# Kernel optimization log

Hardware: AMD Instinct MI355X
Metric: run time of the kernel (lower is better)

Reference implementation:

```python
import jax, jax.numpy as jnp
import numpy as np

DIM = 384
HEADS = 12
HEAD_DIM = DIM // HEADS
SCALE = HEAD_DIM ** -0.5
HIDDEN = 4 * DIM
EPS = 1e-5


def _dwconv(x, w, b):
    # depthwise 3x3 conv, NCHW, kernel [C,1,3,3], groups=C
    y = jax.lax.conv_general_dilated(
        x, w, window_strides=(1, 1), padding='SAME',
        dimension_numbers=('NCHW', 'OIHW', 'NCHW'),
        feature_group_count=x.shape[1])
    return y + b[None, :, None, None]


def _layernorm(x, g, b):
    mu = jnp.mean(x, axis=-1, keepdims=True)
    var = jnp.mean(jnp.square(x - mu), axis=-1, keepdims=True)
    return (x - mu) * jax.lax.rsqrt(var + EPS) * g + b


def setup_inputs() -> dict:
    key = jax.random.key(0)
    ks = jax.random.split(key, 10)
    s = 0.02
    inp = {
        'x': jax.random.normal(ks[0], (32, DIM, 28, 28), dtype=jnp.float32),
        'cpe1_w': jax.random.normal(ks[1], (DIM, 1, 3, 3), dtype=jnp.float32) * s,
        'cpe1_b': jnp.zeros((DIM,), jnp.float32),
        'norm1_g': jnp.ones((DIM,), jnp.float32),
        'norm1_b': jnp.zeros((DIM,), jnp.float32),
        'qkv_w': jax.random.normal(ks[2], (3 * DIM, DIM), dtype=jnp.float32) * s,
        'proj_w': jax.random.normal(ks[3], (DIM, DIM), dtype=jnp.float32) * s,
        'proj_b': jnp.zeros((DIM,), jnp.float32),
        'cpe2_w': jax.random.normal(ks[4], (DIM, 1, 3, 3), dtype=jnp.float32) * s,
        'cpe2_b': jnp.zeros((DIM,), jnp.float32),
        'norm2_g': jnp.ones((DIM,), jnp.float32),
        'norm2_b': jnp.zeros((DIM,), jnp.float32),
        'fc1_w': jax.random.normal(ks[5], (HIDDEN, DIM), dtype=jnp.float32) * s,
        'fc1_b': jnp.zeros((HIDDEN,), jnp.float32),
        'fc2_w': jax.random.normal(ks[6], (DIM, HIDDEN), dtype=jnp.float32) * s,
        'fc2_b': jnp.zeros((DIM,), jnp.float32),
    }
    return inp


def reference(x, cpe1_w, cpe1_b, norm1_g, norm1_b, qkv_w, proj_w, proj_b,
              cpe2_w, cpe2_b, norm2_g, norm2_b, fc1_w, fc1_b, fc2_w, fc2_b):
    B, C, H, W = x.shape
    N = H * W
    # cpe1: depthwise conv residual (act = Identity)
    x = x + _dwconv(x, cpe1_w, cpe1_b)
    x = jnp.transpose(x.reshape(B, C, N), (0, 2, 1))  # [B, N, C]

    # channel attention
    cur = _layernorm(x, norm1_g, norm1_b)
    qkv = cur @ qkv_w.T  # [B, N, 3C]
    qkv = qkv.reshape(B, N, 3, HEADS, HEAD_DIM)
    q = qkv[:, :, 0]  # [B, N, h, d]
    k = qkv[:, :, 1] * SCALE
    v = qkv[:, :, 2]
    # attn = k^T @ v over tokens: [B, h, d, d]
    attn = jnp.einsum('bnhd,bnhe->bhde', k, v)
    attn = jax.nn.softmax(attn, axis=-1)
    # out[n,d] = sum_e attn[d,e] * q[n,e]
    out = jnp.einsum('bhde,bnhe->bnhd', attn, q).reshape(B, N, C)
    cur = out @ proj_w.T + proj_b
    x = x + cur

    # cpe2
    x = jnp.transpose(x, (0, 2, 1)).reshape(B, C, H, W)
    x = x + _dwconv(x, cpe2_w, cpe2_b)

    # MLP
    x = jnp.transpose(x.reshape(B, C, N), (0, 2, 1))  # [B, N, C]
    y = _layernorm(x, norm2_g, norm2_b)
    y = jax.nn.gelu(y @ fc1_w.T + fc1_b, approximate=False)
    y = y @ fc2_w.T + fc2_b
    x = x + y
    return jnp.transpose(x, (0, 2, 1)).reshape(B, C, H, W)
```

## Files before the change

kernel.cpp:

```cpp
#include <hip/hip_runtime.h>
#include <hip/hip_bf16.h>

#define CDIM 384
#define NHEADS 12
#define HDIM 32
#define HIDDEN 1536
#define BBATCH 32
#define HH 28
#define WW 28
#define NTOK 784
#define BN (BBATCH * NTOK)
#define LN_EPS 1e-5f
#define ATT_SCALE 0.17677669529663687f
#define YTILES 196
#define PERXCD 25

typedef __hip_bfloat16 bf16;
typedef __attribute__((ext_vector_type(8))) short bf16x8;
typedef __attribute__((ext_vector_type(4))) float f32x4;

__device__ __forceinline__ float ldf(const float* p) { return *p; }
__device__ __forceinline__ float ldf(const bf16* p) { return __bfloat162float(*p); }
__device__ __forceinline__ void stf(float* p, float v) { *p = v; }
__device__ __forceinline__ void stf(bf16* p, float v) { *p = __float2bfloat16(v); }

__device__ __forceinline__ short f2bs(float v) {
    bf16 t = __float2bfloat16(v);
    return *reinterpret_cast<short*>(&t);
}

__device__ __forceinline__ float gelu_f(float x) {
    float u = x * (0.7978845608f + 0.0356774081f * x * x);
    float e = __expf(-2.f * u);
    return x / (1.f + e);
}

__device__ __forceinline__ void gload16(const void* g, void* l) {
    __builtin_amdgcn_global_load_lds(
        (const __attribute__((address_space(1))) unsigned int*)g,
        (__attribute__((address_space(3))) unsigned int*)l, 16, 0, 0);
}

__global__ __launch_bounds__(256) void f2b4_k(
    const float* __restrict__ w0, const float* __restrict__ w1,
    const float* __restrict__ w2, const float* __restrict__ w3,
    bf16* __restrict__ dst)
{
    int i = blockIdx.x * 256 + threadIdx.x;
    const float* src; int off;
    if (i < 442368)       { src = w0; off = i; }
    else if (i < 589824)  { src = w1; off = i - 442368; }
    else if (i < 1179648) { src = w2; off = i - 589824; }
    else                  { src = w3; off = i - 1179648; }
    dst[i] = __float2bfloat16(src[off]);
}

__global__ __launch_bounds__(256) void wtr_k(const float* __restrict__ w,
                                             float* __restrict__ wt)
{
    int i = blockIdx.x * 256 + threadIdx.x;
    if (i < 9 * CDIM) {
        int k = i / CDIM, c = i % CDIM;
        wt[i] = w[c * 9 + k];
    }
}

__global__ __launch_bounds__(256) void dwconv_nchw_plane(
    const float* __restrict__ x, const float* __restrict__ w,
    const float* __restrict__ bias, float* __restrict__ y)
{
    __shared__ float sm[NTOK];
    int bc = blockIdx.x;
    int c = bc % CDIM;
    const float* xp = x + (size_t)bc * NTOK;
    int tid = threadIdx.x;
#pragma unroll
    for (int i = 0; i < 4; i++) {
        int p = tid + i * 256;
        if (p < NTOK) sm[p] = xp[p];
    }
    __syncthreads();
    const float* wp = w + c * 9;
    float w00 = wp[0], w01 = wp[1], w02 = wp[2];
    float w10 = wp[3], w11 = wp[4], w12 = wp[5];
    float w20 = wp[6], w21 = wp[7], w22 = wp[8];
    float bc_ = bias[c];
    float* yp = y + (size_t)bc * NTOK;
#pragma unroll
    for (int i = 0; i < 4; i++) {
        int p = tid + i * 256;
        if (p >= NTOK) break;
        int h = p / WW, wcol = p % WW;
        bool hm = h > 0, hp = h < HH - 1, wm = wcol > 0, wpv = wcol < WW - 1;
        float s = w11 * sm[p];
        if (hm)        s += w01 * sm[p - WW];
        if (hp)        s += w21 * sm[p + WW];
        if (wm)        s += w10 * sm[p - 1];
        if (wpv)       s += w12 * sm[p + 1];
        if (hm && wm)  s += w00 * sm[p - WW - 1];
        if (hm && wpv) s += w02 * sm[p - WW + 1];
        if (hp && wm)  s += w20 * sm[p + WW - 1];
        if (hp && wpv) s += w22 * sm[p + WW + 1];
        yp[p] = sm[p] + s + bc_;
    }
}

__global__ __launch_bounds__(256) void transpose_in(
    const float* __restrict__ in, float* __restrict__ out)
{
    __shared__ float t[32][33];
    int b = blockIdx.z;
    int n0 = blockIdx.y * 32;
    int c0 = blockIdx.x * 32;
    int tx = threadIdx.x, ty = threadIdx.y;
    for (int i = ty; i < 32; i += 8) {
        int n = n0 + tx;
        if (n < NTOK) t[i][tx] = in[((size_t)b * CDIM + c0 + i) * NTOK + n];
    }
    __syncthreads();
    for (int i = ty; i < 32; i += 8) {
        int n = n0 + i;
        if (n < NTOK) out[((size_t)b * NTOK + n) * CDIM + c0 + tx] = t[tx][i];
    }
}

__global__ __launch_bounds__(256) void dwconv_bnc_v2(
    const float* __restrict__ xin, const float* __restrict__ wt,
    const float* __restrict__ bias, float* __restrict__ xout)
{
    const int nblk = (BN * 96) / 256;
    const int per = nblk >> 3;
    int blk = blockIdx.x;
    int blk2 = (blk & 7) * per + (blk >> 3);
    int g4 = blk2 * 256 + threadIdx.x;
    int q = g4 % 96;
    int r = g4 / 96;
    int c = q * 4;
    int n = r % NTOK, b = r / NTOK;
    int h = n / WW, wcol = n % WW;
    const float4* base = (const float4*)(xin + (size_t)b * NTOK * CDIM);
    bool hm = h > 0, hp = h < HH - 1, wm = wcol > 0, wpv = wcol < WW - 1;

    float4 ctr = base[(size_t)n * 96 + q];
    float4 acc = {0.f, 0.f, 0.f, 0.f};

    const float4* w4 = (const float4*)wt;
#define TAP(k, cond, dn)                                            \
    if (cond) {                                                     \
        float4 vv = base[(size_t)(n + (dn)) * 96 + q];              \
        float4 ww = w4[(k) * 96 + q];                               \
        acc.x = fmaf(ww.x, vv.x, acc.x);                            \
        acc.y = fmaf(ww.y, vv.y, acc.y);                            \
        acc.z = fmaf(ww.z, vv.z, acc.z);                            \
        acc.w = fmaf(ww.w, vv.w, acc.w);                            \
    }
    TAP(0, hm && wm,   -WW - 1)
    TAP(1, hm,         -WW)
    TAP(2, hm && wpv,  -WW + 1)
    TAP(3, wm,         -1)
    { float4 ww = w4[4 * 96 + q];
      acc.x = fmaf(ww.x, ctr.x, acc.x); acc.y = fmaf(ww.y, ctr.y, acc.y);
      acc.z = fmaf(ww.z, ctr.z, acc.z); acc.w = fmaf(ww.w, ctr.w, acc.w); }
    TAP(5, wpv,        1)
    TAP(6, hp && wm,   WW - 1)
    TAP(7, hp,         WW)
    TAP(8, hp && wpv,  WW + 1)
#undef TAP
    float4 bb = *(const float4*)(bias + c);
    float4 outv;
    outv.x = ctr.x + acc.x + bb.x;
    outv.y = ctr.y + acc.y + bb.y;
    outv.z = ctr.z + acc.z + bb.z;
    outv.w = ctr.w + acc.w + bb.w;
    ((float4*)(xout))[g4] = outv;
}

template <typename TO>
__global__ __launch_bounds__(256) void layernorm_k(
    const float* __restrict__ in, const float* __restrict__ g,
    const float* __restrict__ b, TO* __restrict__ out)
{
    int wid = threadIdx.x >> 6;
    int lane = threadIdx.x & 63;
    size_t r = (size_t)blockIdx.x * 4 + wid;
    const float* row = in + r * CDIM;
    float v[6];
    float s = 0.f;
#pragma unroll
    for (int j = 0; j < 6; j++) { v[j] = row[lane + 64 * j]; s += v[j]; }
#pragma unroll
    for (int off = 32; off >= 1; off >>= 1) s += __shfl_xor(s, off);
    float mu = s * (1.f / CDIM);
    float q = 0.f;
#pragma unroll
    for (int j = 0; j < 6; j++) { float d = v[j] - mu; q += d * d; }
#pragma unroll
    for (int off = 32; off >= 1; off >>= 1) q += __shfl_xor(q, off);
    float rs = rsqrtf(q * (1.f / CDIM) + LN_EPS);
    TO* orow = out + r * CDIM;
#pragma unroll
    for (int j = 0; j < 6; j++) {
        int c = lane + 64 * j;
        stf(&orow[c], (v[j] - mu) * rs * g[c] + b[c]);
    }
}

template <int ACT, bool RES, typename TO>
__global__ __launch_bounds__(256, 4) void gemm_mfma(
    const short* __restrict__ Abf, const short* __restrict__ Bw,
    const float* __restrict__ bias, const float* __restrict__ res,
    TO* __restrict__ Co, int K, int M, int NX)
{
    int id = blockIdx.x;
    int xcd = id & 7, slot_ = id >> 3;
    int yloc = slot_ / NX, xx = slot_ - yloc * NX;
    int y = xcd * PERXCD + yloc;
    if (y >= YTILES) return;

    __shared__ __align__(16) short lds[16896];
    const int tid = threadIdx.x;
    const int wid = tid >> 6, lane = tid & 63;
    const int wrow = wid >> 1, wcol = wid & 1;
    const int quad = lane >> 4, lr = lane & 15;
    const int r0 = y * 128, m0 = xx * 128;

    const int srow = lane >> 2;
    const int sg   = (lane & 3) ^ (lane >> 4);
    const short* gA = Abf + (size_t)(r0 + wid * 32 + srow) * K + sg * 8;
    const short* gB = Bw  + (size_t)(m0 + wid * 32 + srow) * K + sg * 8;

    auto stage = [&](int k0, int p) {
        short* lA = lds + p * 8192 + wid * 1024;
        short* lB = lds + p * 8192 + 4096 + wid * 1024;
#pragma unroll
        for (int k = 0; k < 2; k++) {
            gload16(gA + k0 + (size_t)k * 16 * K, lA + k * 512);
            gload16(gB + k0 + (size_t)k * 16 * K, lB + k * 512);
        }
    };

    const int slot = (quad ^ (lr >> 2)) * 8;
    int fAoff[4], fBoff[4];
#pragma unroll
    for (int i = 0; i < 4; i++) {
        fAoff[i] = (wrow * 64 + i * 16 + lr) * 32 + slot;
        fBoff[i] = (wcol * 64 + i * 16 + lr) * 32 + slot;
    }

    f32x4 acc[4][4] = {};

    stage(0, 0);
    int p = 0;
    for (int k0 = 0; k0 < K; k0 += 32) {
        __syncthreads();
        if (k0 + 32 < K) stage(k0 + 32, p ^ 1);
        const short* As = lds + p * 8192;
        const short* Bs = As + 4096;
        bf16x8 av[4], bv[4];
#pragma unroll
        for (int i = 0; i < 4; i++) {
            av[i] = *(const bf16x8*)(As + fAoff[i]);
            bv[i] = *(const bf16x8*)(Bs + fBoff[i]);
        }
#pragma unroll
        for (int i = 0; i < 4; i++)
#pragma unroll
            for (int j = 0; j < 4; j++)
                acc[i][j] = __builtin_amdgcn_mfma_f32_16x16x32_bf16(
                    av[i], bv[j], acc[i][j], 0, 0, 0);
        p ^= 1;
    }

    if constexpr (sizeof(TO) == 4) {
#pragma unroll
        for (int i = 0; i < 4; i++) {
            int gr = r0 + wrow * 64 + i * 16 + quad * 4;
#pragma unroll
            for (int j = 0; j < 4; j++) {
                int gc = m0 + wcol * 64 + j * 16 + lr;
                float bb = bias ? bias[gc] : 0.f;
#pragma unroll
                for (int rr = 0; rr < 4; rr++) {
                    size_t idx = (size_t)(gr + rr) * M + gc;
                    float v = acc[i][j][rr] + bb;
                    if (RES) v += res[idx];
                    if (ACT == 1) v = gelu_f(v);
                    stf((float*)&Co[idx], v);
                }
            }
        }
    } else {
        __syncthreads();
        short* Cs = lds;
#pragma unroll
        for (int i = 0; i < 4; i++) {
            int lrow = wrow * 64 + i * 16 + quad * 4;
#pragma unroll
            for (int j = 0; j < 4; j++) {
                int lcol = wcol * 64 + j * 16 + lr;
                float bb = bias ? bias[m0 + lcol] : 0.f;
#pragma unroll
                for (int rr = 0; rr < 4; rr++) {
                    float v = acc[i][j][rr] + bb;
                    if (ACT == 1) v = gelu_f(v);
                    Cs[(lrow + rr) * 132 + lcol] = f2bs(v);
                }
            }
        }
        __syncthreads();
        short* co = (short*)Co;
#pragma unroll
        for (int s = 0; s < 16; s++) {
            int row = s * 8 + (tid >> 5);
            int seg = tid & 31;
            uint2 vv = *(const uint2*)(Cs + row * 132 + seg * 4);
            *(uint2*)(co + (size_t)(r0 + row) * M + m0 + seg * 4) = vv;
        }
    }
}

__global__ __launch_bounds__(256) void attn_k(
    const bf16* __restrict__ qkv, float* __restrict__ attn)
{
    int bh = blockIdx.x;
    int b = bh / NHEADS, h = bh % NHEADS;
    __shared__ float ks[64][32];
    __shared__ float vs[64][32];
    __shared__ float sm[32][33];
    int tid = threadIdx.x;
    int d = tid >> 3, e0 = (tid & 7) * 4;
    float acc[4] = {0.f, 0.f, 0.f, 0.f};
    for (int n0 = 0; n0 < NTOK; n0 += 64) {
#pragma unroll
        for (int i = 0; i < 8; i++) {
            int idx = tid + i * 256;
            int nn = idx >> 5, cc = idx & 31;
            int n = n0 + nn;
            float kv = 0.f, vv = 0.f;
            if (n < NTOK) {
                size_t base = ((size_t)b * NTOK + n) * (3 * CDIM);
                kv = ATT_SCALE * __bfloat162float(qkv[base + CDIM + h * HDIM + cc]);
                vv = __bfloat162float(qkv[base + 2 * CDIM + h * HDIM + cc]);
            }
            ks[nn][cc] = kv; vs[nn][cc] = vv;
        }
        __syncthreads();
#pragma unroll 8
        for (int nn = 0; nn < 64; nn++) {
            float kd = ks[nn][d];
#pragma unroll
            for (int j = 0; j < 4; j++) acc[j] += kd * vs[nn][e0 + j];
        }
        __syncthreads();
    }
#pragma unroll
    for (int j = 0; j < 4; j++) sm[d][e0 + j] = acc[j];
    __syncthreads();
    if (tid < 32) {
        float mx = -1e30f;
#pragma unroll
        for (int e = 0; e < 32; e++) mx = fmaxf(mx, sm[tid][e]);
        float ssum = 0.f;
        float ex[32];
#pragma unroll
        for (int e = 0; e < 32; e++) { ex[e] = expf(sm[tid][e] - mx); ssum += ex[e]; }
        float inv = 1.f / ssum;
        float* arow = attn + ((size_t)bh * 32 + tid) * 32;
#pragma unroll
        for (int e = 0; e < 32; e++) arow[e] = ex[e] * inv;
    }
}

__global__ __launch_bounds__(384) void apply_attn_k(
    const bf16* __restrict__ qkv, const float* __restrict__ attn,
    bf16* __restrict__ out)
{
    int b = blockIdx.x;
    int chunk = blockIdx.y;
    int tid = threadIdx.x;
    int h = tid >> 5;
    __shared__ float qs[8][CDIM];
    float at[32];
    const float4* ap = (const float4*)(attn + ((size_t)(b * NHEADS) * 32 + tid) * 32);
#pragma unroll
    for (int e4 = 0; e4 < 8; e4++) {
        float4 v = ap[e4];
        at[e4 * 4 + 0] = v.x; at[e4 * 4 + 1] = v.y;
        at[e4 * 4 + 2] = v.z; at[e4 * 4 + 3] = v.w;
    }
    int nbase = chunk * 56;
    for (int t0 = 0; t0 < 56; t0 += 8) {
        __syncthreads();
#pragma unroll
        for (int i = 0; i < 8; i++) {
            int n = nbase + t0 + i;
            qs[i][tid] = __bfloat162float(qkv[((size_t)b * NTOK + n) * (3 * CDIM) + tid]);
        }
        __syncthreads();
#pragma unroll
        for (int i = 0; i < 8; i++) {
            const float* qrow = &qs[i][h * 32];
            float s = 0.f;
#pragma unroll
            for (int e = 0; e < 32; e++) s += at[e] * qrow[e];
            int n = nbase + t0 + i;
            out[((size_t)b * NTOK + n) * CDIM + tid] = __float2bfloat16(s);
        }
    }
}

__global__ __launch_bounds__(256) void transpose_out(
    const float* __restrict__ in, float* __restrict__ out)
{
    __shared__ float t[32][33];
    int b = blockIdx.z;
    int n0 = blockIdx.y * 32;
    int c0 = blockIdx.x * 32;
    int tx = threadIdx.x, ty = threadIdx.y;
    for (int i = ty; i < 32; i += 8) {
        int n = n0 + i;
        if (n < NTOK) t[i][tx] = in[((size_t)b * NTOK + n) * CDIM + c0 + tx];
    }
    __syncthreads();
    for (int i = ty; i < 32; i += 8) {
        int c = c0 + i;
        int n = n0 + tx;
        if (n < NTOK) out[((size_t)b * CDIM + c) * NTOK + n] = t[tx][i];
    }
}

extern "C" void kernel_launch(void* const* d_in, const int* in_sizes, int n_in,
                              void* d_out, int out_size, void* d_ws, size_t ws_size,
                              hipStream_t stream) {
    const float* x      = (const float*)d_in[0];
    const float* cpe1_w = (const float*)d_in[1];
    const float* cpe1_b = (const float*)d_in[2];
    const float* n1g    = (const float*)d_in[3];
    const float* n1b    = (const float*)d_in[4];
    const float* qkv_w  = (const float*)d_in[5];
    const float* proj_w = (const float*)d_in[6];
    const float* proj_b = (const float*)d_in[7];
    const float* cpe2_w = (const float*)d_in[8];
    const float* cpe2_b = (const float*)d_in[9];
    const float* n2g    = (const float*)d_in[10];
    const float* n2b    = (const float*)d_in[11];
    const float* fc1_w  = (const float*)d_in[12];
    const float* fc1_b  = (const float*)d_in[13];
    const float* fc2_w  = (const float*)d_in[14];
    const float* fc2_b  = (const float*)d_in[15];

    const size_t A = (size_t)BN * CDIM;
    const size_t HA = A / 2;

    bf16* wqkv  = (bf16*)d_ws;
    bf16* wproj = wqkv + 442368;
    bf16* wfc1  = wproj + 147456;
    bf16* wfc2  = wfc1 + 589824;
    float* base = (float*)d_ws + 884736;

    float* xt        = base;
    bf16*  curb      = (bf16*)(base + A);
    bf16*  ylnb      = (bf16*)(base + A);
    bf16*  qkvb      = (bf16*)(base + A + HA);
    float* x3        = base + A + HA;
    bf16*  h1        = (bf16*)(base + A + HA + A);
    float* attnm     = base + 3 * A;
    bf16*  attn_outb = (bf16*)(base + 3 * A + 393216);
    float* finalb    = base;
    float* xconv     = base + (A * 7) / 2;
    float* cpe2_wt   = base + (A * 9) / 2;

    const int GEMM_GRID3  = 8 * PERXCD * 3;
    const int GEMM_GRID9  = 8 * PERXCD * 9;
    const int GEMM_GRID12 = 8 * PERXCD * 12;

    f2b4_k<<<1769472 / 256, 256, 0, stream>>>(qkv_w, proj_w, fc1_w, fc2_w, wqkv);
    wtr_k<<<14, 256, 0, stream>>>(cpe2_w, cpe2_wt);

    dwconv_nchw_plane<<<BBATCH * CDIM, 256, 0, stream>>>(x, cpe1_w, cpe1_b, xconv);
    transpose_in<<<dim3(CDIM / 32, (NTOK + 31) / 32, BBATCH), dim3(32, 8), 0, stream>>>(
        xconv, xt);
    layernorm_k<bf16><<<BN / 4, 256, 0, stream>>>(xt, n1g, n1b, curb);
    gemm_mfma<0, false, bf16><<<GEMM_GRID9, 256, 0, stream>>>(
        (const short*)curb, (const short*)wqkv, nullptr, nullptr, qkvb, 384, 1152, 9);
    attn_k<<<BBATCH * NHEADS, 256, 0, stream>>>(qkvb, attnm);
    apply_attn_k<<<dim3(BBATCH, 14), 384, 0, stream>>>(qkvb, attnm, attn_outb);
    gemm_mfma<0, true, float><<<GEMM_GRID3, 256, 0, stream>>>(
        (const short*)attn_outb, (const short*)wproj, proj_b, xt, xt, 384, 384, 3);
    dwconv_bnc_v2<<<(BN * 96) / 256, 256, 0, stream>>>(xt, cpe2_wt, cpe2_b, x3);
    layernorm_k<bf16><<<BN / 4, 256, 0, stream>>>(x3, n2g, n2b, ylnb);
    gemm_mfma<1, false, bf16><<<GEMM_GRID12, 256, 0, stream>>>(
        (const short*)ylnb, (const short*)wfc1, fc1_b, nullptr, h1, 384, 1536, 12);
    gemm_mfma<0, true, float><<<GEMM_GRID3, 256, 0, stream>>>(
        (const short*)h1, (const short*)wfc2, fc2_b, x3, finalb, 1536, 384, 3);
    transpose_out<<<dim3(CDIM / 32, (NTOK + 31) / 32, BBATCH), dim3(32, 8), 0, stream>>>(
        finalb, (float*)d_out);
}
```

Measured before the change: 451.2 us.

## Fuse cpe2 with layernorm, fold output transpose into fc2 GEMM epilogue

Merges the depthwise cpe2 conv with layernorm2 into one kernel that stages the conv weights in LDS, and writes the fc2 GEMM output directly in NCHW through an LDS-staged transposed epilogue, which removes the transpose_out kernel. It also merges the two weight-prep kernels, makes K a template constant, changes the LDS swizzle pattern, and vectorises the inner loops of the attention kernels with float4. The aim is to cut kernel launches and full-tensor round trips through global memory. In exchange, the transposed epilogue adds LDS passes and barriers, and the fused conv reads neighbouring token rows without coalescing them across threads.

```diff
diff --git a/kernel.cpp b/kernel.cpp
--- a/kernel.cpp
+++ b/kernel.cpp
@@ -19,8 +19,6 @@
 typedef __attribute__((ext_vector_type(8))) short bf16x8;
 typedef __attribute__((ext_vector_type(4))) float f32x4;
 
-__device__ __forceinline__ float ldf(const float* p) { return *p; }
-__device__ __forceinline__ float ldf(const bf16* p) { return __bfloat162float(*p); }
 __device__ __forceinline__ void stf(float* p, float v) { *p = v; }
 __device__ __forceinline__ void stf(bf16* p, float v) { *p = __float2bfloat16(v); }
 
@@ -41,28 +39,28 @@
         (__attribute__((address_space(3))) unsigned int*)l, 16, 0, 0);
 }
 
-__global__ __launch_bounds__(256) void f2b4_k(
+__global__ __launch_bounds__(256) void prep_k(
     const float* __restrict__ w0, const float* __restrict__ w1,
     const float* __restrict__ w2, const float* __restrict__ w3,
-    bf16* __restrict__ dst)
-{
-    int i = blockIdx.x * 256 + threadIdx.x;
+    bf16* __restrict__ dst, const float* __restrict__ cw,
+    float* __restrict__ cwt)
+{
+    int blk = blockIdx.x;
+    if (blk >= 6912) {
+        int i = (blk - 6912) * 256 + threadIdx.x;
+        if (i < 9 * CDIM) {
+            int k = i / CDIM, c = i % CDIM;
+            cwt[i] = cw[c * 9 + k];
+        }
+        return;
+    }
+    int i = blk * 256 + threadIdx.x;
     const float* src; int off;
     if (i < 442368)       { src = w0; off = i; }
     else if (i < 589824)  { src = w1; off = i - 442368; }
     else if (i < 1179648) { src = w2; off = i - 589824; }
     else                  { src = w3; off = i - 1179648; }
     dst[i] = __float2bfloat16(src[off]);
-}
-
-__global__ __launch_bounds__(256) void wtr_k(const float* __restrict__ w,
-                                             float* __restrict__ wt)
-{
-    int i = blockIdx.x * 256 + threadIdx.x;
-    if (i < 9 * CDIM) {
-        int k = i / CDIM, c = i % CDIM;
-        wt[i] = w[c * 9 + k];
-    }
 }
 
 __global__ __launch_bounds__(256) void dwconv_nchw_plane(
@@ -124,57 +122,6 @@
     }
 }
 
-__global__ __launch_bounds__(256) void dwconv_bnc_v2(
-    const float* __restrict__ xin, const float* __restrict__ wt,
-    const float* __restrict__ bias, float* __restrict__ xout)
-{
-    const int nblk = (BN * 96) / 256;
-    const int per = nblk >> 3;
-    int blk = blockIdx.x;
-    int blk2 = (blk & 7) * per + (blk >> 3);
-    int g4 = blk2 * 256 + threadIdx.x;
-    int q = g4 % 96;
-    int r = g4 / 96;
-    int c = q * 4;
-    int n = r % NTOK, b = r / NTOK;
-    int h = n / WW, wcol = n % WW;
-    const float4* base = (const float4*)(xin + (size_t)b * NTOK * CDIM);
-    bool hm = h > 0, hp = h < HH - 1, wm = wcol > 0, wpv = wcol < WW - 1;
-
-    float4 ctr = base[(size_t)n * 96 + q];
-    float4 acc = {0.f, 0.f, 0.f, 0.f};
-
-    const float4* w4 = (const float4*)wt;
-#define TAP(k, cond, dn)                                            \
-    if (cond) {                                                     \
-        float4 vv = base[(size_t)(n + (dn)) * 96 + q];              \
-        float4 ww = w4[(k) * 96 + q];                               \
-        acc.x = fmaf(ww.x, vv.x, acc.x);                            \
-        acc.y = fmaf(ww.y, vv.y, acc.y);                            \
-        acc.z = fmaf(ww.z, vv.z, acc.z);                            \
-        acc.w = fmaf(ww.w, vv.w, acc.w);                            \
-    }
-    TAP(0, hm && wm,   -WW - 1)
-    TAP(1, hm,         -WW)
-    TAP(2, hm && wpv,  -WW + 1)
-    TAP(3, wm,         -1)
-    { float4 ww = w4[4 * 96 + q];
-      acc.x = fmaf(ww.x, ctr.x, acc.x); acc.y = fmaf(ww.y, ctr.y, acc.y);
-      acc.z = fmaf(ww.z, ctr.z, acc.z); acc.w = fmaf(ww.w, ctr.w, acc.w); }
-    TAP(5, wpv,        1)
-    TAP(6, hp && wm,   WW - 1)
-    TAP(7, hp,         WW)
-    TAP(8, hp && wpv,  WW + 1)
-#undef TAP
-    float4 bb = *(const float4*)(bias + c);
-    float4 outv;
-    outv.x = ctr.x + acc.x + bb.x;
-    outv.y = ctr.y + acc.y + bb.y;
-    outv.z = ctr.z + acc.z + bb.z;
-    outv.w = ctr.w + acc.w + bb.w;
-    ((float4*)(xout))[g4] = outv;
-}
-
 template <typename TO>
 __global__ __launch_bounds__(256) void layernorm_k(
     const float* __restrict__ in, const float* __restrict__ g,
@@ -205,11 +152,78 @@
     }
 }
 
-template <int ACT, bool RES, typename TO>
+__global__ __launch_bounds__(256) void cpe2_ln_fused(
+    const float* __restrict__ xin, const float* __restrict__ wt,
+    const float* __restrict__ cbias, const float* __restrict__ g,
+    const float* __restrict__ b, float* __restrict__ x3,
+    bf16* __restrict__ lnout)
+{
+    __shared__ float wts[9 * CDIM];
+    int tid = threadIdx.x;
+    for (int i = tid; i < 9 * CDIM; i += 256) wts[i] = wt[i];
+    __syncthreads();
+    int wid = tid >> 6, lane = tid & 63;
+    int tok = blockIdx.x * 4 + wid;
+    int n = tok % NTOK;
+    int h = n / WW, w = n % WW;
+    bool hm = h > 0, hp = h < HH - 1, wm = w > 0, wpv = w < WW - 1;
+    const float* row = xin + (size_t)tok * CDIM;
+    float ctr[6], acc6[6], val[6];
+#pragma unroll
+    for (int j = 0; j < 6; j++) {
+        int c = lane + 64 * j;
+        ctr[j] = row[c];
+        acc6[j] = wts[4 * CDIM + c] * ctr[j];
+    }
+#define TAP(k, cond, dn)                                                      \
+    if (cond) {                                                               \
+        const float* rp = row + (dn) * CDIM;                                  \
+        _Pragma("unroll")                                                     \
+        for (int j = 0; j < 6; j++) {                                         \
+            int c = lane + 64 * j;                                            \
+            acc6[j] = fmaf(wts[(k) * CDIM + c], rp[c], acc6[j]);              \
+        }                                                                     \
+    }
+    TAP(0, hm && wm,   -WW - 1)
+    TAP(1, hm,         -WW)
+    TAP(2, hm && wpv,  -WW + 1)
+    TAP(3, wm,         -1)
+    TAP(5, wpv,        1)
+    TAP(6, hp && wm,   WW - 1)
+    TAP(7, hp,         WW)
+    TAP(8, hp && wpv,  WW + 1)
+#undef TAP
+    float s = 0.f;
+    float* x3row = x3 + (size_t)tok * CDIM;
+#pragma unroll
+    for (int j = 0; j < 6; j++) {
+        int c = lane + 64 * j;
+        val[j] = ctr[j] + acc6[j] + cbias[c];
+        x3row[c] = val[j];
+        s += val[j];
+    }
+#pragma unroll
+    for (int off = 32; off >= 1; off >>= 1) s += __shfl_xor(s, off);
+    float mu = s * (1.f / CDIM);
+    float q = 0.f;
+#pragma unroll
+    for (int j = 0; j < 6; j++) { float d = val[j] - mu; q += d * d; }
+#pragma unroll
+    for (int off = 32; off >= 1; off >>= 1) q += __shfl_xor(q, off);
+    float rs = rsqrtf(q * (1.f / CDIM) + LN_EPS);
+    bf16* orow = lnout + (size_t)tok * CDIM;
+#pragma unroll
+    for (int j = 0; j < 6; j++) {
+        int c = lane + 64 * j;
+        orow[c] = __float2bfloat16((val[j] - mu) * rs * g[c] + b[c]);
+    }
+}
+
+template <int ACT, bool RES, typename TO, bool OUTT, int K>
 __global__ __launch_bounds__(256, 4) void gemm_mfma(
     const short* __restrict__ Abf, const short* __restrict__ Bw,
     const float* __restrict__ bias, const float* __restrict__ res,
-    TO* __restrict__ Co, int K, int M, int NX)
+    TO* __restrict__ Co, int M, int NX)
 {
     int id = blockIdx.x;
     int xcd = id & 7, slot_ = id >> 3;
@@ -225,7 +239,7 @@
     const int r0 = y * 128, m0 = xx * 128;
 
     const int srow = lane >> 2;
-    const int sg   = (lane & 3) ^ (lane >> 4);
+    const int sg   = (lane & 3) ^ ((lane >> 3) & 3);
     const short* gA = Abf + (size_t)(r0 + wid * 32 + srow) * K + sg * 8;
     const short* gB = Bw  + (size_t)(m0 + wid * 32 + srow) * K + sg * 8;
 
@@ -239,12 +253,12 @@
         }
     };
 
-    const int slot = (quad ^ (lr >> 2)) * 8;
-    int fAoff[4], fBoff[4];
+    const int slot = (quad ^ ((lr >> 1) & 3)) * 8;
+    int fA[4], fB[4];
 #pragma unroll
     for (int i = 0; i < 4; i++) {
-        fAoff[i] = (wrow * 64 + i * 16 + lr) * 32 + slot;
-        fBoff[i] = (wcol * 64 + i * 16 + lr) * 32 + slot;
+        fA[i] = (wrow * 64 + i * 16 + lr) * 32 + slot;
+        fB[i] = 4096 + (wcol * 64 + i * 16 + lr) * 32 + slot;
     }
 
     f32x4 acc[4][4] = {};
@@ -255,12 +269,11 @@
         __syncthreads();
         if (k0 + 32 < K) stage(k0 + 32, p ^ 1);
         const short* As = lds + p * 8192;
-        const short* Bs = As + 4096;
         bf16x8 av[4], bv[4];
 #pragma unroll
         for (int i = 0; i < 4; i++) {
-            av[i] = *(const bf16x8*)(As + fAoff[i]);
-            bv[i] = *(const bf16x8*)(Bs + fBoff[i]);
+            av[i] = *(const bf16x8*)(As + fA[i]);
+            bv[i] = *(const bf16x8*)(As + fB[i]);
         }
 #pragma unroll
         for (int i = 0; i < 4; i++)
@@ -271,7 +284,46 @@
         p ^= 1;
     }
 
-    if constexpr (sizeof(TO) == 4) {
+    if constexpr (OUTT) {
+        float* Csf = (float*)lds;
+        __syncthreads();
+#pragma unroll
+        for (int pass = 0; pass < 2; pass++) {
+            if (wcol == pass) {
+#pragma unroll
+                for (int i = 0; i < 4; i++) {
+                    int lrow = wrow * 64 + i * 16 + quad * 4;
+#pragma unroll
+                    for (int j = 0; j < 4; j++) {
+                        int lcol = j * 16 + lr;
+                        int gc = m0 + pass * 64 + lcol;
+                        float bb = bias ? bias[gc] : 0.f;
+#pragma unroll
+                        for (int rr = 0; rr < 4; rr++) {
+                            float v = acc[i][j][rr] + bb;
+                            if (RES)
+                                v += res[(size_t)(r0 + lrow + rr) * M + gc];
+                            if (ACT == 1) v = gelu_f(v);
+                            Csf[(lrow + rr) * 66 + lcol] = v;
+                        }
+                    }
+                }
+            }
+            __syncthreads();
+            int tok = tid & 127;
+            int csel = tid >> 7;
+            int gtok = r0 + tok;
+            int bb2 = gtok / NTOK;
+            int nn2 = gtok - bb2 * NTOK;
+#pragma unroll
+            for (int s = 0; s < 32; s++) {
+                int cl = s * 2 + csel;
+                int gcol = m0 + pass * 64 + cl;
+                Co[((size_t)bb2 * CDIM + gcol) * NTOK + nn2] = Csf[tok * 66 + cl];
+            }
+            __syncthreads();
+        }
+    } else if constexpr (sizeof(TO) == 4) {
 #pragma unroll
         for (int i = 0; i < 4; i++) {
             int gr = r0 + wrow * 64 + i * 16 + quad * 4;
@@ -348,8 +400,11 @@
 #pragma unroll 8
         for (int nn = 0; nn < 64; nn++) {
             float kd = ks[nn][d];
-#pragma unroll
-            for (int j = 0; j < 4; j++) acc[j] += kd * vs[nn][e0 + j];
+            float4 vv4 = *(const float4*)&vs[nn][e0];
+            acc[0] = fmaf(kd, vv4.x, acc[0]);
+            acc[1] = fmaf(kd, vv4.y, acc[1]);
+            acc[2] = fmaf(kd, vv4.z, acc[2]);
+            acc[3] = fmaf(kd, vv4.w, acc[3]);
         }
         __syncthreads();
     }
@@ -399,33 +454,19 @@
         __syncthreads();
 #pragma unroll
         for (int i = 0; i < 8; i++) {
-            const float* qrow = &qs[i][h * 32];
+            const float4* q4 = (const float4*)&qs[i][h * 32];
             float s = 0.f;
 #pragma unroll
-            for (int e = 0; e < 32; e++) s += at[e] * qrow[e];
+            for (int e4 = 0; e4 < 8; e4++) {
+                float4 qv = q4[e4];
+                s = fmaf(at[e4 * 4 + 0], qv.x, s);
+                s = fmaf(at[e4 * 4 + 1], qv.y, s);
+                s = fmaf(at[e4 * 4 + 2], qv.z, s);
+                s = fmaf(at[e4 * 4 + 3], qv.w, s);
+            }
             int n = nbase + t0 + i;
             out[((size_t)b * NTOK + n) * CDIM + tid] = __float2bfloat16(s);
         }
-    }
-}
-
-__global__ __launch_bounds__(256) void transpose_out(
-    const float* __restrict__ in, float* __restrict__ out)
-{
-    __shared__ float t[32][33];
-    int b = blockIdx.z;
-    int n0 = blockIdx.y * 32;
-    int c0 = blockIdx.x * 32;
-    int tx = threadIdx.x, ty = threadIdx.y;
-    for (int i = ty; i < 32; i += 8) {
-        int n = n0 + i;
-        if (n < NTOK) t[i][tx] = in[((size_t)b * NTOK + n) * CDIM + c0 + tx];
-    }
-    __syncthreads();
-    for (int i = ty; i < 32; i += 8) {
-        int c = c0 + i;
-        int n = n0 + tx;
-        if (n < NTOK) out[((size_t)b * CDIM + c) * NTOK + n] = t[tx][i];
     }
 }
 
@@ -466,7 +507,6 @@
     bf16*  h1        = (bf16*)(base + A + HA + A);
     float* attnm     = base + 3 * A;
     bf16*  attn_outb = (bf16*)(base + 3 * A + 393216);
-    float* finalb    = base;
     float* xconv     = base + (A * 7) / 2;
     float* cpe2_wt   = base + (A * 9) / 2;
 
@@ -474,25 +514,23 @@
     const int GEMM_GRID9  = 8 * PERXCD * 9;
     const int GEMM_GRID12 = 8 * PERXCD * 12;
 
-    f2b4_k<<<1769472 / 256, 256, 0, stream>>>(qkv_w, proj_w, fc1_w, fc2_w, wqkv);
-    wtr_k<<<14, 256, 0, stream>>>(cpe2_w, cpe2_wt);
+    prep_k<<<6926, 256, 0, stream>>>(qkv_w, proj_w, fc1_w, fc2_w, wqkv,
+                                     cpe2_w, cpe2_wt);
 
     dwconv_nchw_plane<<<BBATCH * CDIM, 256, 0, stream>>>(x, cpe1_w, cpe1_b, xconv);
     transpose_in<<<dim3(CDIM / 32, (NTOK + 31) / 32, BBATCH), dim3(32, 8), 0, stream>>>(
         xconv, xt);
     layernorm_k<bf16><<<BN / 4, 256, 0, stream>>>(xt, n1g, n1b, curb);
-    gemm_mfma<0, false, bf16><<<GEMM_GRID9, 256, 0, stream>>>(
-        (const short*)curb, (const short*)wqkv, nullptr, nullptr, qkvb, 384, 1152, 9);
+    gemm_mfma<0, false, bf16, false, 384><<<GEMM_GRID9, 256, 0, stream>>>(
+        (const short*)curb, (const short*)wqkv, nullptr, nullptr, qkvb, 1152, 9);
     attn_k<<<BBATCH * NHEADS, 256, 0, stream>>>(qkvb, attnm);
     apply_attn_k<<<dim3(BBATCH, 14), 384, 0, stream>>>(qkvb, attnm, attn_outb);
-    gemm_mfma<0, true, float><<<GEMM_GRID3, 256, 0, stream>>>(
-        (const short*)attn_outb, (const short*)wproj, proj_b, xt, xt, 384, 384, 3);
-    dwconv_bnc_v2<<<(BN * 96) / 256, 256, 0, stream>>>(xt, cpe2_wt, cpe2_b, x3);
-    layernorm_k<bf16><<<BN / 4, 256, 0, stream>>>(x3, n2g, n2b, ylnb);
-    gemm_mfma<1, false, bf16><<<GEMM_GRID12, 256, 0, stream>>>(
-        (const short*)ylnb, (const short*)wfc1, fc1_b, nullptr, h1, 384, 1536, 12);
-    gemm_mfma<0, true, float><<<GEMM_GRID3, 256, 0, stream>>>(
-        (const short*)h1, (const short*)wfc2, fc2_b, x3, finalb, 1536, 384, 3);
-    transpose_out<<<dim3(CDIM / 32, (NTOK + 31) / 32, BBATCH), dim3(32, 8), 0, stream>>>(
-        finalb, (float*)d_out);
-}
+    gemm_mfma<0, true, float, false, 384><<<GEMM_GRID3, 256, 0, stream>>>(
+        (const short*)attn_outb, (const short*)wproj, proj_b, xt, xt, 384, 3);
+    cpe2_ln_fused<<<BN / 4, 256, 0, stream>>>(xt, cpe2_wt, cpe2_b, n2g, n2b,
+                                              x3, ylnb);
+    gemm_mfma<1, false, bf16, false, 384><<<GEMM_GRID12, 256, 0, stream>>>(
+        (const short*)ylnb, (const short*)wfc1, fc1_b, nullptr, h1, 1536, 12);
+    gemm_mfma<0, true, float, true, 1536><<<GEMM_GRID3, 256, 0, stream>>>(
+        (const short*)h1, (const short*)wfc2, fc2_b, x3, (float*)d_out, 384, 3);
+}
```

Result: faster. 438.5 us (-2.8%).
